# Optimization experiments

Hardware: AMD Instinct MI355X
Metric: run time of the kernel (lower is better)

Reference implementation:

```python
import jax, jax.numpy as jnp
import numpy as np

B, N, M = 64, 256, 16
ONF, OEF = 92, 41
NF, EF = 128, 64
FINAL = 128  # final_node_len; final_layer outputs FINAL//2


def _linear_params(key, fan_in, fan_out):
    # kaiming_uniform fan_in, relu: bound = sqrt(6/fan_in)
    bound = np.sqrt(6.0 / fan_in)
    W = jax.random.uniform(key, (fan_out, fan_in), jnp.float32, -bound, bound)
    b = jnp.zeros((fan_out,), jnp.float32)
    return W, b


def setup_inputs() -> dict:
    key = jax.random.key(0)
    ks = jax.random.split(key, 12)
    node_fea = jax.random.normal(ks[0], (B, N, ONF), jnp.float32)
    edge_fea = jax.random.normal(ks[1], (B, N, M, OEF), jnp.float32)
    edge_fea_idx = jax.random.randint(ks[2], (B, N, M), 0, N)
    dis = jax.random.uniform(ks[3], (N, N), jnp.float32)
    Wn, bn = _linear_params(ks[4], ONF, NF)
    We, be = _linear_params(ks[5], OEF, EF)
    W1, b1 = _linear_params(ks[6], 2 * NF + EF, 2 * NF)
    W2, b2 = _linear_params(ks[7], 2 * NF + EF, 2 * NF)
    W3, b3 = _linear_params(ks[8], 2 * NF + EF, 2 * NF)
    Wf, bf = _linear_params(ks[9], NF, FINAL // 2)
    return dict(node_fea=node_fea, edge_fea=edge_fea, edge_fea_idx=edge_fea_idx,
                dis=dis, Wn=Wn, bn=bn, We=We, be=be,
                W1=W1, b1=b1, a1=jnp.float32(0.7),
                W2=W2, b2=b2, a2=jnp.float32(0.7),
                W3=W3, b3=b3, a3=jnp.float32(0.7),
                Wf=Wf, bf=bf,
                DAw=jnp.float32(48.0 / 5.0), DAb=jnp.float32(-28.0 / 5.0))


def _conv(nf, ef, idx, W, b, alpha):
    # nf: [B,N,F]; ef: [B,N,M,E]; idx: [B,N,M]
    Bb, Nn, Mm = idx.shape
    F = nf.shape[-1]
    idx_c = jnp.maximum(idx, 0)
    gathered = jax.vmap(lambda x, i: x[i])(nf, idx_c)           # [B,N,M,F]
    self_exp = jnp.broadcast_to(nf[:, :, None, :], (Bb, Nn, Mm, F))
    total = jnp.concatenate([self_exp, gathered, ef], axis=-1)   # [B,N,M,2F+E]
    gated = jnp.einsum('bnmi,oi->bnmo', total, W) + b            # [B,N,M,2F]
    nbr_filter, nbr_core = jnp.split(gated, 2, axis=-1)
    mask = (idx >= 0).astype(nf.dtype)[..., None]
    nbr_filter = jax.nn.sigmoid(nbr_filter) * mask
    nbr_core = jax.nn.softplus(nbr_core)
    nbr_sumed = jnp.sum(nbr_filter * nbr_core, axis=2)           # [B,N,F]
    return jax.nn.softplus(alpha * nf + nbr_sumed)


def reference(node_fea, edge_fea, edge_fea_idx, dis,
              Wn, bn, We, be,
              W1, b1, a1, W2, b2, a2, W3, b3, a3,
              Wf, bf, DAw, DAb):
    nf = node_fea @ Wn.T + bn                                    # [B,N,NF]
    ef = edge_fea @ We.T + be                                    # [B,N,M,EF]
    nf = _conv(nf, ef, edge_fea_idx, W1, b1, a1)
    nf = _conv(nf, ef, edge_fea_idx, W2, b2, a2)
    nf = _conv(nf, ef, edge_fea_idx, W3, b3, a3)
    nf = nf @ Wf.T + bf                                          # [B,N,FINAL//2]
    DA = jax.nn.sigmoid(DAw * dis + DAb)                         # [N,N]
    node1 = jnp.einsum('ij,bjf->bif', DA, nf)
    return jnp.concatenate([nf, node1], axis=2)                  # [B,N,FINAL]
```

## Files before the change

### kernel.cpp

```cpp
#include <hip/hip_runtime.h>
#include <hip/hip_bf16.h>
#include <math.h>

#define Bb   64
#define Nn   256
#define Mm   16
#define ONF  92
#define OEF  41
#define NF   128
#define EF   64
#define KDIM 320
#define ODIM 256
#define FINAL 128
#define K0C  6

#define LOG2E_F 1.44269504088896f
#define LN2_F   0.6931471805599453f

typedef __attribute__((ext_vector_type(8))) short short8;
typedef __attribute__((ext_vector_type(4))) float f32x4;

__device__ __forceinline__ float sigmoidf_(float x) {
    float e = __expf(-x);
    return __builtin_amdgcn_rcpf(1.0f + e);
}
__device__ __forceinline__ float softplusf_(float x) {
    return fmaxf(x, 0.0f) + __logf(1.0f + __expf(-fabsf(x)));
}
__device__ __forceinline__ __hip_bfloat16 to_bf16(float x) { return __float2bfloat16(x); }

__device__ __forceinline__ void swz(const float* __restrict__ in, __hip_bfloat16* __restrict__ out,
                                    int t, int Itot, int koff, int Kuse, int K0, float scale)
{
    int j = t & 7;
    int u = t >> 3;
    int lane = u & 63;
    int ln16 = lane & 15, q = lane >> 4;
    int v = u >> 6;
    int k0 = v % K0, tile = v / K0;
    int n = tile * 16 + ln16, k = k0 * 32 + q * 8 + j;
    out[t] = (k < Kuse) ? to_bf16(scale * in[(size_t)n * Itot + koff + k]) : to_bf16(0.0f);
}

#define SZ_WET (OEF * EF)
#define SZ_WB  (16 * K0C * 512)
#define SZ_WS  (16 * 4 * 512)
#define SZ_WNB ((NF / 16) * 3 * 512)
#define SZ_WEB ((EF / 16) * 2 * 512)
#define SZ_WFB ((64 / 16) * 4 * 512)
#define SZ_DA  (Nn * Nn)
#define PREP_TOTAL (SZ_WET + 3 * SZ_WB + 3 * SZ_WS + SZ_WNB + SZ_WEB + SZ_WFB + SZ_DA)

__global__ __launch_bounds__(256) void k_prep(
    const float* __restrict__ We, const float* __restrict__ W1,
    const float* __restrict__ W2, const float* __restrict__ W3,
    const float* __restrict__ Wn, const float* __restrict__ Wf,
    const float* __restrict__ dis, const float* __restrict__ pw, const float* __restrict__ pb,
    float* __restrict__ WeT,
    __hip_bfloat16* __restrict__ W1b, __hip_bfloat16* __restrict__ W2b, __hip_bfloat16* __restrict__ W3b,
    __hip_bfloat16* __restrict__ W1s, __hip_bfloat16* __restrict__ W2s, __hip_bfloat16* __restrict__ W3s,
    __hip_bfloat16* __restrict__ Wnb, __hip_bfloat16* __restrict__ Web, __hip_bfloat16* __restrict__ Wfb,
    __hip_bfloat16* __restrict__ DAf)
{
    int t = blockIdx.x * 256 + threadIdx.x;
    if (t < SZ_WET) {
        int o = t / OEF, i = t - o * OEF;
        WeT[i * EF + o] = We[t];
        return;
    }
    t -= SZ_WET;
    if (t < SZ_WB) { swz(W1, W1b, t, KDIM, NF, 192, K0C, LOG2E_F); return; }
    t -= SZ_WB;
    if (t < SZ_WB) { swz(W2, W2b, t, KDIM, NF, 192, K0C, LOG2E_F); return; }
    t -= SZ_WB;
    if (t < SZ_WB) { swz(W3, W3b, t, KDIM, NF, 192, K0C, LOG2E_F); return; }
    t -= SZ_WB;
    if (t < SZ_WS) { swz(W1, W1s, t, KDIM, 0, NF, 4, LOG2E_F); return; }
    t -= SZ_WS;
    if (t < SZ_WS) { swz(W2, W2s, t, KDIM, 0, NF, 4, LOG2E_F); return; }
    t -= SZ_WS;
    if (t < SZ_WS) { swz(W3, W3s, t, KDIM, 0, NF, 4, LOG2E_F); return; }
    t -= SZ_WS;
    if (t < SZ_WNB) { swz(Wn, Wnb, t, ONF, 0, ONF, 3, 1.0f); return; }
    t -= SZ_WNB;
    if (t < SZ_WEB) { swz(We, Web, t, OEF, 0, OEF, 2, 1.0f); return; }
    t -= SZ_WEB;
    if (t < SZ_WFB) { swz(Wf, Wfb, t, NF, 0, NF, 4, 1.0f); return; }
    t -= SZ_WFB;
    if (t < SZ_DA) {
        int i = t >> 8, jx = t & 255;
        float v = sigmoidf_(fmaf(*pw, dis[t], *pb));
        int itile = i >> 4, ln16 = i & 15;
        int k0 = jx >> 5, q = (jx >> 3) & 3, jj = jx & 7;
        DAf[(size_t)((((itile * 8 + k0) << 6) + (q << 4) + ln16)) * 8 + jj] = to_bf16(v);
    }
}

template<int KIN, int K0, int NCOLS>
__device__ __forceinline__ void emb_body(
    int bid, const float* __restrict__ X, const __hip_bfloat16* __restrict__ Bswz,
    const float* __restrict__ bias, __hip_bfloat16* __restrict__ Y,
    __hip_bfloat16* A_s, __hip_bfloat16* O_s)
{
    constexpr int KP = K0 * 32;
    constexpr int TPW = NCOLS / 64;
    constexpr int OLD = NCOLS + 24;

    const int row0 = bid * 64;
    const int t = threadIdx.x;

    {
        const float4* Xb = (const float4*)(X + (size_t)row0 * KIN);
        constexpr int NV = (64 * KIN) / 4;
        for (int c = t; c < NV; c += 256) {
            float4 v = Xb[c];
            int flat = c * 4;
            #pragma unroll
            for (int e = 0; e < 4; e++) {
                int f = flat + e;
                int row = f / KIN, k = f - row * KIN;
                int mt = row >> 4, ln16 = row & 15;
                int k0 = k >> 5, q = (k >> 3) & 3, j = k & 7;
                float vv = (e == 0) ? v.x : (e == 1) ? v.y : (e == 2) ? v.z : v.w;
                A_s[(((mt * K0 + k0) << 6) + (q << 4) + ln16) * 8 + j] = to_bf16(vv);
            }
        }
        constexpr int PAD = KP - KIN;
        for (int c = t; c < 64 * PAD; c += 256) {
            int row = c / PAD, k = KIN + (c - row * PAD);
            int mt = row >> 4, ln16 = row & 15;
            int k0 = k >> 5, q = (k >> 3) & 3, j = k & 7;
            A_s[(((mt * K0 + k0) << 6) + (q << 4) + ln16) * 8 + j] = to_bf16(0.0f);
        }
    }
    __syncthreads();

    const int wv = t >> 6, lane = t & 63;
    const int q = lane >> 4, ln16 = lane & 15;

    f32x4 acc[4][TPW];
    #pragma unroll
    for (int p = 0; p < TPW; p++) {
        float bv = bias[(wv * TPW + p) * 16 + ln16];
        #pragma unroll
        for (int mt = 0; mt < 4; mt++) acc[mt][p] = (f32x4){bv, bv, bv, bv};
    }

    short8 bw[TPW][K0];
    #pragma unroll
    for (int p = 0; p < TPW; p++)
        #pragma unroll
        for (int k0 = 0; k0 < K0; k0++)
            bw[p][k0] = *(const short8*)(Bswz + ((size_t)((wv * TPW + p) * K0 + k0) << 9) + (lane << 3));

    #pragma unroll
    for (int k0 = 0; k0 < K0; k0++) {
        short8 af[4];
        #pragma unroll
        for (int mt = 0; mt < 4; mt++)
            af[mt] = *(const short8*)(A_s + (((mt * K0 + k0) << 6) + lane) * 8);
        #pragma unroll
        for (int mt = 0; mt < 4; mt++)
            #pragma unroll
            for (int p = 0; p < TPW; p++)
                acc[mt][p] = __builtin_amdgcn_mfma_f32_16x16x32_bf16(af[mt], bw[p][k0], acc[mt][p], 0, 0, 0);
    }

    #pragma unroll
    for (int mt = 0; mt < 4; mt++)
        #pragma unroll
        for (int p = 0; p < TPW; p++) {
            int col = (wv * TPW + p) * 16 + ln16;
            #pragma unroll
            for (int r = 0; r < 4; r++)
                O_s[(mt * 16 + q * 4 + r) * OLD + col] = to_bf16(acc[mt][p][r]);
        }
    __syncthreads();
    constexpr int CH = NCOLS / 8;
    for (int c = t; c < 64 * CH; c += 256) {
        int row = c / CH, ch = c - row * CH;
        *(uint4*)(Y + (size_t)(row0 + row) * NCOLS + ch * 8) =
            *(const uint4*)(O_s + row * OLD + ch * 8);
    }
}

__global__ __launch_bounds__(256) void k_embed_all(
    const float* __restrict__ node_fea, const __hip_bfloat16* __restrict__ Wnb,
    const float* __restrict__ bn, __hip_bfloat16* __restrict__ nf0,
    const float* __restrict__ edge_fea, const __hip_bfloat16* __restrict__ Web,
    const float* __restrict__ be, __hip_bfloat16* __restrict__ efb)
{
    __shared__ __align__(16) __hip_bfloat16 A_s[4 * 3 * 512];
    __shared__ __align__(16) __hip_bfloat16 O_s[64 * (NF + 24)];
    if (blockIdx.x < 256)
        emb_body<ONF, 3, NF>(blockIdx.x, node_fea, Wnb, bn, nf0, A_s, O_s);
    else
        emb_body<OEF, 2, EF>(blockIdx.x - 256, edge_fea, Web, be, efb, A_s, O_s);
}

template<bool PRECOMP>
__global__ __launch_bounds__(256, 3) void k_conv_mfma(
    const __hip_bfloat16* __restrict__ nf_in,
    const float* __restrict__ edge_fea,
    const __hip_bfloat16* __restrict__ ef_bf,
    const int*   __restrict__ eidx,
    const float* __restrict__ WeT,
    const float* __restrict__ be,
    const __hip_bfloat16* __restrict__ Wb,
    const __hip_bfloat16* __restrict__ Wsb,
    const float* __restrict__ bias,
    const float* __restrict__ palpha,
    __hip_bfloat16* __restrict__ nf_out)
{
    __shared__ __align__(16) __hip_bfloat16 A_s[4 * K0C * 512];
    __shared__ __align__(16) __hip_bfloat16 A_sf[4 * 512];

    const int node0 = blockIdx.x * 4;
    const int b = node0 >> 8;
    const int t = threadIdx.x;
    const int wv = t >> 6, lane = t & 63;
    const int q = lane >> 4, ln16 = lane & 15;
    const int row = (wv << 4) + ln16;

    const int myidx = eidx[node0 * Mm + row];
    const unsigned long long mball = __ballot(eidx[node0 * Mm + lane] >= 0);

    float selfv[8];
    #pragma unroll
    for (int mt = 0; mt < 4; mt++)
        #pragma unroll
        for (int p = 0; p < 2; p++)
            selfv[mt * 2 + p] =
                __bfloat162float(nf_in[(size_t)(node0 + mt) * NF + (2 * wv + p) * 16 + ln16]);

    {
        int j = myidx < 0 ? 0 : myidx;
        const __hip_bfloat16* gathp = nf_in + (size_t)((b << 8) + j) * NF;
        #pragma unroll
        for (int k0 = 0; k0 < 4; k0++)
            *(uint4*)(A_s + ((wv * K0C + k0) * 64 + lane) * 8) =
                *(const uint4*)(gathp + k0 * 32 + q * 8);
        *(uint4*)(A_sf + (wv * 64 + lane) * 8) =
            *(const uint4*)(nf_in + (size_t)(node0 + (ln16 & 3)) * NF + wv * 32 + q * 8);
        if (PRECOMP) {
            const __hip_bfloat16* efp = ef_bf + (size_t)((node0 << 4) + row) * EF;
            #pragma unroll
            for (int k0 = 0; k0 < 2; k0++)
                *(uint4*)(A_s + ((wv * K0C + 4 + k0) * 64 + lane) * 8) =
                    *(const uint4*)(efp + k0 * 32 + q * 8);
        } else {
            for (int c = t; c < 64 * EF; c += 256) {
                int rr = c >> 6, col = c & 63;
                float a = be[col];
                const float* er = edge_fea + (size_t)(node0 * Mm + rr) * OEF;
                #pragma unroll
                for (int i = 0; i < OEF; i++) a = fmaf(er[i], WeT[i * EF + col], a);
                int mt = rr >> 4, l16 = rr & 15;
                int k0 = 4 + (col >> 5), qq = (col >> 3) & 3, jj = col & 7;
                A_s[((mt * K0C + k0) * 64 + qq * 16 + l16) * 8 + jj] = to_bf16(a);
            }
        }
    }
    __syncthreads();

    f32x4 sv[4];
    #pragma unroll
    for (int c = 0; c < 4; c++) {
        int tile = 2 * wv + (c & 1) + ((c >> 1) << 3);
        float bv = bias[tile * 16 + ln16] * LOG2E_F;
        sv[c] = (f32x4){bv, bv, bv, bv};
    }
    #pragma unroll
    for (int k0 = 0; k0 < 4; k0++) {
        short8 afs = *(const short8*)(A_sf + (k0 * 64 + lane) * 8);
        #pragma unroll
        for (int c = 0; c < 4; c++) {
            int tile = 2 * wv + (c & 1) + ((c >> 1) << 3);
            short8 bws = *(const short8*)(Wsb + ((size_t)(tile * 4 + k0) << 9) + (lane << 3));
            sv[c] = __builtin_amdgcn_mfma_f32_16x16x32_bf16(afs, bws, sv[c], 0, 0, 0);
        }
    }

    f32x4 accF[4][2], accC[4][2];
    #pragma unroll
    for (int mt = 0; mt < 4; mt++) {
        #pragma unroll
        for (int p = 0; p < 2; p++) {
            float vF = __shfl(sv[p][mt], ln16);
            float vC = __shfl(sv[2 + p][mt], ln16);
            accF[mt][p] = (f32x4){vF, vF, vF, vF};
            accC[mt][p] = (f32x4){vC, vC, vC, vC};
        }
    }

    const __hip_bfloat16* WF0 = Wb + ((size_t)(2 * wv) * (K0C * 512)) + (lane << 3);
    const __hip_bfloat16* WF1 = WF0 + K0C * 512;
    const __hip_bfloat16* WC0 = WF0 + 8 * (K0C * 512);
    const __hip_bfloat16* WC1 = WC0 + K0C * 512;

    #pragma unroll
    for (int k0 = 0; k0 < K0C; k0++) {
        short8 cF0 = *(const short8*)(WF0 + k0 * 512);
        short8 cF1 = *(const short8*)(WF1 + k0 * 512);
        short8 cC0 = *(const short8*)(WC0 + k0 * 512);
        short8 cC1 = *(const short8*)(WC1 + k0 * 512);
        short8 af[4];
        #pragma unroll
        for (int mt = 0; mt < 4; mt++)
            af[mt] = *(const short8*)(A_s + ((mt * K0C + k0) * 64 + lane) * 8);
        #pragma unroll
        for (int mt = 0; mt < 4; mt++) {
            accF[mt][0] = __builtin_amdgcn_mfma_f32_16x16x32_bf16(af[mt], cF0, accF[mt][0], 0, 0, 0);
            accF[mt][1] = __builtin_amdgcn_mfma_f32_16x16x32_bf16(af[mt], cF1, accF[mt][1], 0, 0, 0);
            accC[mt][0] = __builtin_amdgcn_mfma_f32_16x16x32_bf16(af[mt], cC0, accC[mt][0], 0, 0, 0);
            accC[mt][1] = __builtin_amdgcn_mfma_f32_16x16x32_bf16(af[mt], cC1, accC[mt][1], 0, 0, 0);
        }
    }

    const float alpha = *palpha;
    #pragma unroll
    for (int mt = 0; mt < 4; mt++) {
        const int gnode = node0 + mt;
        unsigned mbits = (unsigned)(mball >> (mt * 16 + q * 4)) & 0xFu;
        #pragma unroll
        for (int p = 0; p < 2; p++) {
            float partial = 0.0f;
            #pragma unroll
            for (int r = 0; r < 4; r++) {
                bool msk = (mbits >> r) & 1u;
                float f2 = accF[mt][p][r];
                float c2 = accC[mt][p][r];
                float sig = __builtin_amdgcn_rcpf(1.0f + __builtin_amdgcn_exp2f(-f2));
                float sp2 = fmaxf(c2, 0.0f) +
                            __builtin_amdgcn_logf(1.0f + __builtin_amdgcn_exp2f(-fabsf(c2)));
                partial += msk ? sig * sp2 : 0.0f;
            }
            partial += __shfl_xor(partial, 16);
            partial += __shfl_xor(partial, 32);
            if (q == 0) {
                int col = (2 * wv + p) * 16 + ln16;
                nf_out[(size_t)gnode * NF + col] =
                    to_bf16(softplusf_(fmaf(alpha, selfv[mt * 2 + p], LN2_F * partial)));
            }
        }
    }
}

__global__ __launch_bounds__(256) void k_final_mfma(
    const __hip_bfloat16* __restrict__ nf, const __hip_bfloat16* __restrict__ Wfb,
    const float* __restrict__ bfv, float* __restrict__ out,
    __hip_bfloat16* __restrict__ XT)
{
    __shared__ __align__(16) __hip_bfloat16 A_s[16 * 512];
    const int node0 = blockIdx.x * 64;
    const int bloc = node0 >> 8;
    const int t = threadIdx.x;
    const int wv = t >> 6, lane = t & 63;
    const int q = lane >> 4, ln16 = lane & 15;

    const __hip_bfloat16* rowp = nf + (size_t)(node0 + (wv << 4) + ln16) * NF;
    #pragma unroll
    for (int k0 = 0; k0 < 4; k0++)
        *(uint4*)(A_s + ((wv * 4 + k0) * 64 + lane) * 8) =
            *(const uint4*)(rowp + k0 * 32 + q * 8);
    __syncthreads();

    short8 bw[4];
    #pragma unroll
    for (int k0 = 0; k0 < 4; k0++)
        bw[k0] = *(const short8*)(Wfb + ((size_t)(wv * 4 + k0) * 64 + lane) * 8);

    float bv = bfv[wv * 16 + ln16];
    f32x4 acc[4];
    #pragma unroll
    for (int mt = 0; mt < 4; mt++) acc[mt] = (f32x4){bv, bv, bv, bv};

    #pragma unroll
    for (int k0 = 0; k0 < 4; k0++) {
        short8 af[4];
        #pragma unroll
        for (int mt = 0; mt < 4; mt++)
            af[mt] = *(const short8*)(A_s + ((mt * 4 + k0) * 64 + lane) * 8);
        #pragma unroll
        for (int mt = 0; mt < 4; mt++)
            acc[mt] = __builtin_amdgcn_mfma_f32_16x16x32_bf16(af[mt], bw[k0], acc[mt], 0, 0, 0);
    }

    const int col = (wv << 4) + ln16;
    #pragma unroll
    for (int mt = 0; mt < 4; mt++)
        #pragma unroll
        for (int r = 0; r < 4; r++) {
            int row = mt * 16 + q * 4 + r;
            float v = acc[mt][r];
            out[(size_t)(node0 + row) * FINAL + col] = v;
            XT[(size_t)(bloc * 64 + col) * 256 + (node0 & 255) + row] = to_bf16(v);
        }
}

__global__ __launch_bounds__(256) void k_node1_mfma(
    const __hip_bfloat16* __restrict__ DAf,
    const __hip_bfloat16* __restrict__ XT,
    float* __restrict__ out)
{
    __shared__ __align__(16) __hip_bfloat16 B_s[32 * 512];
    const int blk = blockIdx.x;
    const int b = blk >> 2, i0 = (blk & 3) * 64;
    const int t = threadIdx.x;
    const int wv = t >> 6, lane = t & 63;
    const int q = lane >> 4, ln16 = lane & 15;

    const __hip_bfloat16* xrow = XT + (size_t)(b * 64 + (wv << 4) + ln16) * 256;
    #pragma unroll
    for (int k0 = 0; k0 < 8; k0++)
        *(uint4*)(B_s + ((wv * 8 + k0) * 64 + lane) * 8) =
            *(const uint4*)(xrow + k0 * 32 + q * 8);
    __syncthreads();

    f32x4 acc[4];
    #pragma unroll
    for (int mt = 0; mt < 4; mt++) acc[mt] = (f32x4){0.f, 0.f, 0.f, 0.f};

    #pragma unroll
    for (int k0 = 0; k0 < 8; k0++) {
        short8 bfr = *(const short8*)(B_s + ((wv * 8 + k0) * 64 + lane) * 8);
        short8 af[4];
        #pragma unroll
        for (int mt = 0; mt < 4; mt++)
            af[mt] = *(const short8*)(DAf + (size_t)(((i0 >> 4) + mt) * 8 + k0) * 512 + (lane << 3));
        #pragma unroll
        for (int mt = 0; mt < 4; mt++)
            acc[mt] = __builtin_amdgcn_mfma_f32_16x16x32_bf16(af[mt], bfr, acc[mt], 0, 0, 0);
    }

    #pragma unroll
    for (int mt = 0; mt < 4; mt++)
        #pragma unroll
        for (int r = 0; r < 4; r++) {
            int i = i0 + mt * 16 + q * 4 + r;
            out[(size_t)((b << 8) + i) * FINAL + 64 + (wv << 4) + ln16] = acc[mt][r];
        }
}

extern "C" void kernel_launch(void* const* d_in, const int* in_sizes, int n_in,
                              void* d_out, int out_size, void* d_ws, size_t ws_size,
                              hipStream_t stream)
{
    const float* node_fea = (const float*)d_in[0];
    const float* edge_fea = (const float*)d_in[1];
    const int*   eidx     = (const int*)  d_in[2];
    const float* dis      = (const float*)d_in[3];
    const float* Wn = (const float*)d_in[4];
    const float* bn = (const float*)d_in[5];
    const float* We = (const float*)d_in[6];
    const float* be = (const float*)d_in[7];
    const float* W1 = (const float*)d_in[8];
    const float* b1 = (const float*)d_in[9];
    const float* a1 = (const float*)d_in[10];
    const float* W2 = (const float*)d_in[11];
    const float* b2 = (const float*)d_in[12];
    const float* a2 = (const float*)d_in[13];
    const float* W3 = (const float*)d_in[14];
    const float* b3 = (const float*)d_in[15];
    const float* a3 = (const float*)d_in[16];
    const float* Wf = (const float*)d_in[17];
    const float* bf = (const float*)d_in[18];
    const float* DAw = (const float*)d_in[19];
    const float* DAb = (const float*)d_in[20];
    float* out = (float*)d_out;

    char* base = (char*)d_ws;
    size_t off = 0;
    auto alloc = [&](size_t bytes) { char* p = base + off; off = (off + bytes + 255) & ~(size_t)255; return p; };
    __hip_bfloat16* nfA = (__hip_bfloat16*)alloc((size_t)Bb * Nn * NF * 2);
    __hip_bfloat16* nfB = (__hip_bfloat16*)alloc((size_t)Bb * Nn * NF * 2);
    __hip_bfloat16* W1b = (__hip_bfloat16*)alloc((size_t)SZ_WB * 2);
    __hip_bfloat16* W2b = (__hip_bfloat16*)alloc((size_t)SZ_WB * 2);
    __hip_bfloat16* W3b = (__hip_bfloat16*)alloc((size_t)SZ_WB * 2);
    __hip_bfloat16* W1s = (__hip_bfloat16*)alloc((size_t)SZ_WS * 2);
    __hip_bfloat16* W2s = (__hip_bfloat16*)alloc((size_t)SZ_WS * 2);
    __hip_bfloat16* W3s = (__hip_bfloat16*)alloc((size_t)SZ_WS * 2);
    float* WeT = (float*)alloc((size_t)OEF * EF * 4);
    __hip_bfloat16* DAf = (__hip_bfloat16*)alloc((size_t)Nn * Nn * 2);
    __hip_bfloat16* Wnb = (__hip_bfloat16*)alloc((size_t)SZ_WNB * 2);
    __hip_bfloat16* Web = (__hip_bfloat16*)alloc((size_t)SZ_WEB * 2);
    __hip_bfloat16* Wfb = (__hip_bfloat16*)alloc((size_t)SZ_WFB * 2);
    __hip_bfloat16* XT  = (__hip_bfloat16*)alloc((size_t)Bb * 64 * Nn * 2);
    __hip_bfloat16* efb = (__hip_bfloat16*)alloc((size_t)Bb * Nn * Mm * EF * 2);
    const bool precomp = (ws_size >= off);

    hipLaunchKernelGGL(k_prep, dim3((PREP_TOTAL + 255) / 256), dim3(256), 0, stream,
                       We, W1, W2, W3, Wn, Wf, dis, DAw, DAb,
                       WeT, W1b, W2b, W3b, W1s, W2s, W3s, Wnb, Web, Wfb, DAf);

    hipLaunchKernelGGL(k_embed_all, dim3(precomp ? (256 + Bb * Nn * Mm / 64) : 256), dim3(256), 0, stream,
                       node_fea, Wnb, bn, nfA, edge_fea, Web, be, efb);

    if (precomp) {
        hipLaunchKernelGGL((k_conv_mfma<true>), dim3(Bb * Nn / 4), dim3(256), 0, stream,
                           nfA, edge_fea, efb, eidx, WeT, be, W1b, W1s, b1, a1, nfB);
        hipLaunchKernelGGL((k_conv_mfma<true>), dim3(Bb * Nn / 4), dim3(256), 0, stream,
                           nfB, edge_fea, efb, eidx, WeT, be, W2b, W2s, b2, a2, nfA);
        hipLaunchKernelGGL((k_conv_mfma<true>), dim3(Bb * Nn / 4), dim3(256), 0, stream,
                           nfA, edge_fea, efb, eidx, WeT, be, W3b, W3s, b3, a3, nfB);
    } else {
        hipLaunchKernelGGL((k_conv_mfma<false>), dim3(Bb * Nn / 4), dim3(256), 0, stream,
                           nfA, edge_fea, efb, eidx, WeT, be, W1b, W1s, b1, a1, nfB);
        hipLaunchKernelGGL((k_conv_mfma<false>), dim3(Bb * Nn / 4), dim3(256), 0, stream,
                           nfB, edge_fea, efb, eidx, WeT, be, W2b, W2s, b2, a2, nfA);
        hipLaunchKernelGGL((k_conv_mfma<false>), dim3(Bb * Nn / 4), dim3(256), 0, stream,
                           nfA, edge_fea, efb, eidx, WeT, be, W3b, W3s, b3, a3, nfB);
    }

    hipLaunchKernelGGL(k_final_mfma, dim3(Bb * Nn / 64), dim3(256), 0, stream, nfB, Wfb, bf, out, XT);
    hipLaunchKernelGGL(k_node1_mfma, dim3(Bb * 4), dim3(256), 0, stream, DAf, XT, out);
}
```

Baseline: 298.3 us.

## Add persistent multi-group conv kernel with register-resident weights and double-buffered LDS staging

```diff
diff --git a/kernel.cpp b/kernel.cpp
--- a/kernel.cpp
+++ b/kernel.cpp
@@ -13,12 +13,22 @@
 #define ODIM 256
 #define FINAL 128
 #define K0C  6
+#define GRP  8
+#define NODESB (4*GRP)
 
 #define LOG2E_F 1.44269504088896f
 #define LN2_F   0.6931471805599453f
 
 typedef __attribute__((ext_vector_type(8))) short short8;
 typedef __attribute__((ext_vector_type(4))) float f32x4;
+
+#define AS1 __attribute__((address_space(1)))
+#define AS3 __attribute__((address_space(3)))
+
+__device__ __forceinline__ void gl2lds16(const void* gp, void* lp) {
+    __builtin_amdgcn_global_load_lds((AS1 void*)(void*)gp, (AS3 void*)lp, 16, 0, 0);
+}
+#define KEEP8(x) asm volatile("" : "+v"(x))
 
 __device__ __forceinline__ float sigmoidf_(float x) {
     float e = __expf(-x);
@@ -198,6 +208,171 @@
         emb_body<OEF, 2, EF>(blockIdx.x - 256, edge_fea, Web, be, efb, A_s, O_s);
 }
 
+__global__ __launch_bounds__(256, 2) void k_conv_blk(
+    const __hip_bfloat16* __restrict__ nf_in,
+    const __hip_bfloat16* __restrict__ ef_bf,
+    const int*   __restrict__ eidx,
+    const __hip_bfloat16* __restrict__ Wb,
+    const __hip_bfloat16* __restrict__ Wsb,
+    const float* __restrict__ bias,
+    const float* __restrict__ palpha,
+    __hip_bfloat16* __restrict__ nf_out)
+{
+    __shared__ __align__(16) __hip_bfloat16 A_s[2][4 * K0C * 512];
+    __shared__ __align__(16) __hip_bfloat16 A_sf[8 * 512];
+
+    const int node0_blk = blockIdx.x * NODESB;
+    const int bbase = node0_blk & ~255;
+    const int t = threadIdx.x;
+    const int wv = t >> 6, lane = t & 63;
+    const int q = lane >> 4, ln16 = lane & 15;
+    const int row = (wv << 4) + ln16;
+    const float alpha = *palpha;
+
+    auto stage_group = [&](int node0g, __hip_bfloat16* buf) -> unsigned long long {
+        int mi = eidx[node0g * Mm + row];
+        unsigned long long mb = __ballot(eidx[node0g * Mm + lane] >= 0);
+        int j = mi < 0 ? 0 : mi;
+        const __hip_bfloat16* gathp = nf_in + (size_t)(bbase + j) * NF + q * 8;
+        #pragma unroll
+        for (int k0 = 0; k0 < 4; k0++)
+            gl2lds16(gathp + k0 * 32, buf + (wv * K0C + k0) * 512 + lane * 8);
+        const __hip_bfloat16* efp = ef_bf + (size_t)((node0g << 4) + row) * EF + q * 8;
+        #pragma unroll
+        for (int k0 = 0; k0 < 2; k0++)
+            gl2lds16(efp + k0 * 32, buf + (wv * K0C + 4 + k0) * 512 + lane * 8);
+        return mb;
+    };
+
+    {
+        const __hip_bfloat16* s0 = nf_in + (size_t)(node0_blk + ln16) * NF + wv * 32 + q * 8;
+        gl2lds16(s0, A_sf + wv * 512 + lane * 8);
+        gl2lds16(s0 + (size_t)16 * NF, A_sf + (4 + wv) * 512 + lane * 8);
+    }
+    unsigned long long mb_next = stage_group(node0_blk, A_s[0]);
+    __syncthreads();
+
+    const __hip_bfloat16* WF0 = Wb + ((size_t)(2 * wv) * (K0C * 512)) + (lane << 3);
+    const __hip_bfloat16* WF1 = WF0 + K0C * 512;
+    const __hip_bfloat16* WC0 = WF0 + 8 * (K0C * 512);
+    const __hip_bfloat16* WC1 = WC0 + K0C * 512;
+    short8 mF0[K0C], mF1[K0C], mC0[K0C], mC1[K0C];
+    #pragma unroll
+    for (int k0 = 0; k0 < K0C; k0++) {
+        mF0[k0] = *(const short8*)(WF0 + k0 * 512);
+        mF1[k0] = *(const short8*)(WF1 + k0 * 512);
+        mC0[k0] = *(const short8*)(WC0 + k0 * 512);
+        mC1[k0] = *(const short8*)(WC1 + k0 * 512);
+    }
+
+    f32x4 sv0[4], sv1[4];
+    #pragma unroll
+    for (int c = 0; c < 4; c++) {
+        int tile = 2 * wv + (c & 1) + ((c >> 1) << 3);
+        float bv = bias[tile * 16 + ln16] * LOG2E_F;
+        sv0[c] = (f32x4){bv, bv, bv, bv};
+        sv1[c] = (f32x4){bv, bv, bv, bv};
+    }
+    #pragma unroll
+    for (int k0 = 0; k0 < 4; k0++) {
+        short8 af0 = *(const short8*)(A_sf + (k0 * 64 + lane) * 8);
+        short8 af1 = *(const short8*)(A_sf + ((4 + k0) * 64 + lane) * 8);
+        #pragma unroll
+        for (int c = 0; c < 4; c++) {
+            int tile = 2 * wv + (c & 1) + ((c >> 1) << 3);
+            short8 bws = *(const short8*)(Wsb + ((size_t)(tile * 4 + k0) << 9) + (lane << 3));
+            sv0[c] = __builtin_amdgcn_mfma_f32_16x16x32_bf16(af0, bws, sv0[c], 0, 0, 0);
+            sv1[c] = __builtin_amdgcn_mfma_f32_16x16x32_bf16(af1, bws, sv1[c], 0, 0, 0);
+        }
+    }
+
+    #pragma unroll
+    for (int k0 = 0; k0 < K0C; k0++) {
+        KEEP8(mF0[k0]); KEEP8(mF1[k0]); KEEP8(mC0[k0]); KEEP8(mC1[k0]);
+    }
+
+    int cur = 0;
+    #pragma unroll 2
+    for (int g = 0; g < GRP; g++) {
+        const int node0g = node0_blk + g * 4;
+        const unsigned long long mb_cur = mb_next;
+        if (g + 1 < GRP) mb_next = stage_group(node0g + 4, A_s[cur ^ 1]);
+
+        float selfv[8];
+        #pragma unroll
+        for (int mt = 0; mt < 4; mt++)
+            #pragma unroll
+            for (int p = 0; p < 2; p++)
+                selfv[mt * 2 + p] =
+                    __bfloat162float(nf_in[(size_t)(node0g + mt) * NF + (2 * wv + p) * 16 + ln16]);
+
+        const bool gHi = (g >= 4);
+        const int srcl = ((g & 3) << 4) + ln16;
+        const __hip_bfloat16* Acur = A_s[cur];
+
+        #pragma unroll
+        for (int h = 0; h < 2; h++) {
+            f32x4 accF[2][2], accC[2][2];
+            #pragma unroll
+            for (int mtl = 0; mtl < 2; mtl++) {
+                const int mt = 2 * h + mtl;
+                #pragma unroll
+                for (int p = 0; p < 2; p++) {
+                    float sF = gHi ? sv1[p][mt]     : sv0[p][mt];
+                    float sC = gHi ? sv1[2 + p][mt] : sv0[2 + p][mt];
+                    float vF = __shfl(sF, srcl);
+                    float vC = __shfl(sC, srcl);
+                    accF[mtl][p] = (f32x4){vF, vF, vF, vF};
+                    accC[mtl][p] = (f32x4){vC, vC, vC, vC};
+                }
+            }
+            #pragma unroll
+            for (int k0 = 0; k0 < K0C; k0++) {
+                short8 af[2];
+                #pragma unroll
+                for (int mtl = 0; mtl < 2; mtl++)
+                    af[mtl] = *(const short8*)(Acur + (((2 * h + mtl) * K0C + k0) * 64 + lane) * 8);
+                #pragma unroll
+                for (int mtl = 0; mtl < 2; mtl++) {
+                    accF[mtl][0] = __builtin_amdgcn_mfma_f32_16x16x32_bf16(af[mtl], mF0[k0], accF[mtl][0], 0, 0, 0);
+                    accF[mtl][1] = __builtin_amdgcn_mfma_f32_16x16x32_bf16(af[mtl], mF1[k0], accF[mtl][1], 0, 0, 0);
+                    accC[mtl][0] = __builtin_amdgcn_mfma_f32_16x16x32_bf16(af[mtl], mC0[k0], accC[mtl][0], 0, 0, 0);
+                    accC[mtl][1] = __builtin_amdgcn_mfma_f32_16x16x32_bf16(af[mtl], mC1[k0], accC[mtl][1], 0, 0, 0);
+                }
+            }
+            #pragma unroll
+            for (int mtl = 0; mtl < 2; mtl++) {
+                const int mt = 2 * h + mtl;
+                const int gnode = node0g + mt;
+                unsigned mbits = (unsigned)(mb_cur >> (mt * 16 + q * 4)) & 0xFu;
+                #pragma unroll
+                for (int p = 0; p < 2; p++) {
+                    float partial = 0.0f;
+                    #pragma unroll
+                    for (int r = 0; r < 4; r++) {
+                        bool msk = (mbits >> r) & 1u;
+                        float f2 = accF[mtl][p][r];
+                        float c2 = accC[mtl][p][r];
+                        float sig = __builtin_amdgcn_rcpf(1.0f + __builtin_amdgcn_exp2f(-f2));
+                        float sp2 = fmaxf(c2, 0.0f) +
+                                    __builtin_amdgcn_logf(1.0f + __builtin_amdgcn_exp2f(-fabsf(c2)));
+                        partial += msk ? sig * sp2 : 0.0f;
+                    }
+                    partial += __shfl_xor(partial, 16);
+                    partial += __shfl_xor(partial, 32);
+                    if (q == 0) {
+                        int col = (2 * wv + p) * 16 + ln16;
+                        nf_out[(size_t)gnode * NF + col] =
+                            to_bf16(softplusf_(fmaf(alpha, selfv[mt * 2 + p], LN2_F * partial)));
+                    }
+                }
+            }
+        }
+        __syncthreads();
+        cur ^= 1;
+    }
+}
+
 template<bool PRECOMP>
 __global__ __launch_bounds__(256, 3) void k_conv_mfma(
     const __hip_bfloat16* __restrict__ nf_in,
@@ -497,12 +672,12 @@
                        node_fea, Wnb, bn, nfA, edge_fea, Web, be, efb);
 
     if (precomp) {
-        hipLaunchKernelGGL((k_conv_mfma<true>), dim3(Bb * Nn / 4), dim3(256), 0, stream,
-                           nfA, edge_fea, efb, eidx, WeT, be, W1b, W1s, b1, a1, nfB);
-        hipLaunchKernelGGL((k_conv_mfma<true>), dim3(Bb * Nn / 4), dim3(256), 0, stream,
-                           nfB, edge_fea, efb, eidx, WeT, be, W2b, W2s, b2, a2, nfA);
-        hipLaunchKernelGGL((k_conv_mfma<true>), dim3(Bb * Nn / 4), dim3(256), 0, stream,
-                           nfA, edge_fea, efb, eidx, WeT, be, W3b, W3s, b3, a3, nfB);
+        hipLaunchKernelGGL(k_conv_blk, dim3(Bb * Nn / NODESB), dim3(256), 0, stream,
+                           nfA, efb, eidx, W1b, W1s, b1, a1, nfB);
+        hipLaunchKernelGGL(k_conv_blk, dim3(Bb * Nn / NODESB), dim3(256), 0, stream,
+                           nfB, efb, eidx, W2b, W2s, b2, a2, nfA);
+        hipLaunchKernelGGL(k_conv_blk, dim3(Bb * Nn / NODESB), dim3(256), 0, stream,
+                           nfA, efb, eidx, W3b, W3s, b3, a3, nfB);
     } else {
         hipLaunchKernelGGL((k_conv_mfma<false>), dim3(Bb * Nn / 4), dim3(256), 0, stream,
                            nfA, edge_fea, efb, eidx, WeT, be, W1b, W1s, b1, a1, nfB);
```

Measured after the change: 291.5 us. 2.3% less time.

## Split conv linear into per-node projections plus per-edge edge GEMM

Applied to the files above, without the earlier changes.

```diff
diff --git a/kernel.cpp b/kernel.cpp
--- a/kernel.cpp
+++ b/kernel.cpp
@@ -19,6 +19,16 @@
 
 typedef __attribute__((ext_vector_type(8))) short short8;
 typedef __attribute__((ext_vector_type(4))) float f32x4;
+typedef unsigned int uint;
+typedef unsigned short ushort;
+
+#define AS1 __attribute__((address_space(1)))
+#define AS3 __attribute__((address_space(3)))
+
+__device__ __forceinline__ void gl2lds16(const void* gp, void* lp) {
+    __builtin_amdgcn_global_load_lds((AS1 void*)(void*)gp, (AS3 void*)lp, 16, 0, 0);
+}
+#define KEEP8(x) asm volatile("" : "+v"(x))
 
 __device__ __forceinline__ float sigmoidf_(float x) {
     float e = __expf(-x);
@@ -28,6 +38,12 @@
     return fmaxf(x, 0.0f) + __logf(1.0f + __expf(-fabsf(x)));
 }
 __device__ __forceinline__ __hip_bfloat16 to_bf16(float x) { return __float2bfloat16(x); }
+__device__ __forceinline__ float lo16(uint u) { return __uint_as_float(u << 16); }
+__device__ __forceinline__ float hi16(uint u) { return __uint_as_float(u & 0xffff0000u); }
+__device__ __forceinline__ ushort bfbits(float x) {
+    __hip_bfloat16 b = __float2bfloat16(x);
+    return *(ushort*)&b;
+}
 
 __device__ __forceinline__ void swz(const float* __restrict__ in, __hip_bfloat16* __restrict__ out,
                                     int t, int Itot, int koff, int Kuse, int K0, float scale)
@@ -45,11 +61,12 @@
 #define SZ_WET (OEF * EF)
 #define SZ_WB  (16 * K0C * 512)
 #define SZ_WS  (16 * 4 * 512)
+#define SZ_WE2 (16 * 2 * 512)
 #define SZ_WNB ((NF / 16) * 3 * 512)
 #define SZ_WEB ((EF / 16) * 2 * 512)
 #define SZ_WFB ((64 / 16) * 4 * 512)
 #define SZ_DA  (Nn * Nn)
-#define PREP_TOTAL (SZ_WET + 3 * SZ_WB + 3 * SZ_WS + SZ_WNB + SZ_WEB + SZ_WFB + SZ_DA)
+#define PREP_TOTAL (SZ_WET + 3 * SZ_WB + 3 * SZ_WS + SZ_WNB + SZ_WEB + SZ_WFB + 3 * SZ_WS + 3 * SZ_WE2 + SZ_DA)
 
 __global__ __launch_bounds__(256) void k_prep(
     const float* __restrict__ We, const float* __restrict__ W1,
@@ -60,6 +77,8 @@
     __hip_bfloat16* __restrict__ W1b, __hip_bfloat16* __restrict__ W2b, __hip_bfloat16* __restrict__ W3b,
     __hip_bfloat16* __restrict__ W1s, __hip_bfloat16* __restrict__ W2s, __hip_bfloat16* __restrict__ W3s,
     __hip_bfloat16* __restrict__ Wnb, __hip_bfloat16* __restrict__ Web, __hip_bfloat16* __restrict__ Wfb,
+    __hip_bfloat16* __restrict__ W1g, __hip_bfloat16* __restrict__ W2g, __hip_bfloat16* __restrict__ W3g,
+    __hip_bfloat16* __restrict__ W1e2, __hip_bfloat16* __restrict__ W2e2, __hip_bfloat16* __restrict__ W3e2,
     __hip_bfloat16* __restrict__ DAf)
 {
     int t = blockIdx.x * 256 + threadIdx.x;
@@ -87,6 +106,18 @@
     t -= SZ_WEB;
     if (t < SZ_WFB) { swz(Wf, Wfb, t, NF, 0, NF, 4, 1.0f); return; }
     t -= SZ_WFB;
+    if (t < SZ_WS) { swz(W1, W1g, t, KDIM, NF, NF, 4, LOG2E_F); return; }
+    t -= SZ_WS;
+    if (t < SZ_WS) { swz(W2, W2g, t, KDIM, NF, NF, 4, LOG2E_F); return; }
+    t -= SZ_WS;
+    if (t < SZ_WS) { swz(W3, W3g, t, KDIM, NF, NF, 4, LOG2E_F); return; }
+    t -= SZ_WS;
+    if (t < SZ_WE2) { swz(W1, W1e2, t, KDIM, 2 * NF, EF, 2, LOG2E_F); return; }
+    t -= SZ_WE2;
+    if (t < SZ_WE2) { swz(W2, W2e2, t, KDIM, 2 * NF, EF, 2, LOG2E_F); return; }
+    t -= SZ_WE2;
+    if (t < SZ_WE2) { swz(W3, W3e2, t, KDIM, 2 * NF, EF, 2, LOG2E_F); return; }
+    t -= SZ_WE2;
     if (t < SZ_DA) {
         int i = t >> 8, jx = t & 255;
         float v = sigmoidf_(fmaf(*pw, dis[t], *pb));
@@ -196,6 +227,177 @@
         emb_body<ONF, 3, NF>(blockIdx.x, node_fea, Wnb, bn, nf0, A_s, O_s);
     else
         emb_body<OEF, 2, EF>(blockIdx.x - 256, edge_fea, Web, be, efb, A_s, O_s);
+}
+
+__global__ __launch_bounds__(256) void k_gemm_p(
+    const __hip_bfloat16* __restrict__ nf,
+    const __hip_bfloat16* __restrict__ Ws,
+    const __hip_bfloat16* __restrict__ Wg,
+    const float* __restrict__ bias,
+    __hip_bfloat16* __restrict__ P)
+{
+    __shared__ __align__(16) __hip_bfloat16 A_s[8 * 512];
+    const int row0 = blockIdx.x * 32;
+    const int t = threadIdx.x;
+    const int wv = t >> 6, lane = t & 63;
+    const int q = lane >> 4, ln16 = lane & 15;
+
+    #pragma unroll
+    for (int cc = 0; cc < 2; cc++) {
+        int c = 2 * wv + cc;
+        int mt = c >> 2, k0 = c & 3;
+        gl2lds16(nf + (size_t)(row0 + mt * 16 + ln16) * NF + k0 * 32 + q * 8,
+                 (char*)A_s + (size_t)(c * 64 + lane) * 16);
+    }
+    __syncthreads();
+
+    const __hip_bfloat16* wbase = (wv < 2) ? Ws : Wg;
+    f32x4 acc[2][8];
+    #pragma unroll
+    for (int p = 0; p < 8; p++) {
+        float bv = (wv < 2) ? bias[(wv * 8 + p) * 16 + ln16] * LOG2E_F : 0.0f;
+        acc[0][p] = (f32x4){bv, bv, bv, bv};
+        acc[1][p] = (f32x4){bv, bv, bv, bv};
+    }
+
+    #pragma unroll
+    for (int k0 = 0; k0 < 4; k0++) {
+        short8 af0 = *(const short8*)(A_s + ((0 * 4 + k0) * 64 + lane) * 8);
+        short8 af1 = *(const short8*)(A_s + ((1 * 4 + k0) * 64 + lane) * 8);
+        #pragma unroll
+        for (int p = 0; p < 8; p++) {
+            int tt = (wv & 1) * 8 + p;
+            short8 bw = *(const short8*)(wbase + ((size_t)(tt * 4 + k0) << 9) + (lane << 3));
+            acc[0][p] = __builtin_amdgcn_mfma_f32_16x16x32_bf16(af0, bw, acc[0][p], 0, 0, 0);
+            acc[1][p] = __builtin_amdgcn_mfma_f32_16x16x32_bf16(af1, bw, acc[1][p], 0, 0, 0);
+        }
+    }
+
+    #pragma unroll
+    for (int mt = 0; mt < 2; mt++)
+        #pragma unroll
+        for (int p = 0; p < 8; p++) {
+            int col = (wv * 8 + p) * 16 + ln16;
+            #pragma unroll
+            for (int r = 0; r < 4; r++)
+                P[(size_t)(row0 + mt * 16 + q * 4 + r) * 512 + col] = to_bf16(acc[mt][p][r]);
+        }
+}
+
+__global__ __launch_bounds__(256, 3) void k_conv_p(
+    const __hip_bfloat16* __restrict__ nf_in,
+    const __hip_bfloat16* __restrict__ efb,
+    const int*   __restrict__ eidx,
+    const __hip_bfloat16* __restrict__ P,
+    const __hip_bfloat16* __restrict__ Wedge,
+    const float* __restrict__ palpha,
+    __hip_bfloat16* __restrict__ nf_out)
+{
+    __shared__ uint EG[64 * 129];
+    const int node0_blk = blockIdx.x * 16;
+    const int bbase = node0_blk & ~255;
+    const int t = threadIdx.x;
+    const int wv = t >> 6, lane = t & 63;
+    const int q = lane >> 4, ln16 = lane & 15;
+    const float alpha = *palpha;
+
+    short8 ws[4][2];
+    #pragma unroll
+    for (int c = 0; c < 4; c++) {
+        int ct = ((c >> 1) << 3) + 2 * wv + (c & 1);
+        #pragma unroll
+        for (int k0 = 0; k0 < 2; k0++)
+            ws[c][k0] = *(const short8*)(Wedge + ((size_t)(ct * 2 + k0) << 9) + (lane << 3));
+    }
+    #pragma unroll
+    for (int c = 0; c < 4; c++) { KEEP8(ws[c][0]); KEEP8(ws[c][1]); }
+
+    for (int g = 0; g < 4; g++) {
+        const int node0g = node0_blk + g * 4;
+
+        short8 bfr[4][2];
+        #pragma unroll
+        for (int et = 0; et < 4; et++)
+            #pragma unroll
+            for (int k0 = 0; k0 < 2; k0++)
+                bfr[et][k0] = *(const short8*)(
+                    efb + (size_t)((node0g + et) * 16 + ln16) * EF + k0 * 32 + q * 8);
+
+        f32x4 acc[4][4];
+        #pragma unroll
+        for (int et = 0; et < 4; et++)
+            #pragma unroll
+            for (int c = 0; c < 4; c++) acc[et][c] = (f32x4){0.f, 0.f, 0.f, 0.f};
+
+        #pragma unroll
+        for (int k0 = 0; k0 < 2; k0++)
+            #pragma unroll
+            for (int et = 0; et < 4; et++)
+                #pragma unroll
+                for (int c = 0; c < 4; c++)
+                    acc[et][c] = __builtin_amdgcn_mfma_f32_16x16x32_bf16(
+                        ws[c][k0], bfr[et][k0], acc[et][c], 0, 0, 0);
+
+        #pragma unroll
+        for (int et = 0; et < 4; et++) {
+            const int e = et * 16 + ln16;
+            #pragma unroll
+            for (int c = 0; c < 4; c++) {
+                int ct = ((c >> 1) << 3) + 2 * wv + (c & 1);
+                int wbase0 = e * 129 + ct * 8 + q * 2;
+                uint u0 = (uint)bfbits(acc[et][c][0]) | ((uint)bfbits(acc[et][c][1]) << 16);
+                uint u1 = (uint)bfbits(acc[et][c][2]) | ((uint)bfbits(acc[et][c][3]) << 16);
+                EG[wbase0] = u0;
+                EG[wbase0 + 1] = u1;
+            }
+        }
+        __syncthreads();
+
+        {
+            const int n = node0g + wv;
+            const uint* EGrow = EG + (wv * 16) * 129 + lane;
+            uint psF = *(const uint*)(P + (size_t)n * 512 + 2 * lane);
+            uint psC = *(const uint*)(P + (size_t)n * 512 + 128 + 2 * lane);
+            uint sfv = *(const uint*)(nf_in + (size_t)n * NF + 2 * lane);
+            float psFlo = lo16(psF), psFhi = hi16(psF);
+            float psClo = lo16(psC), psChi = hi16(psC);
+            float plo = 0.0f, phi = 0.0f;
+            const int4* ip = (const int4*)(eidx + n * Mm);
+            #pragma unroll
+            for (int mm = 0; mm < 4; mm++) {
+                int4 iv = ip[mm];
+                #pragma unroll
+                for (int k = 0; k < 4; k++) {
+                    int im = (k == 0) ? iv.x : (k == 1) ? iv.y : (k == 2) ? iv.z : iv.w;
+                    int m = mm * 4 + k;
+                    bool msk = im >= 0;
+                    int jm = msk ? im : 0;
+                    const __hip_bfloat16* pg = P + (size_t)(bbase + jm) * 512 + 256;
+                    uint pgF = *(const uint*)(pg + 2 * lane);
+                    uint pgC = *(const uint*)(pg + 128 + 2 * lane);
+                    uint egF = EGrow[m * 129];
+                    uint egC = EGrow[m * 129 + 64];
+                    float flo = lo16(egF) + lo16(pgF) + psFlo;
+                    float fhi = hi16(egF) + hi16(pgF) + psFhi;
+                    float clo = lo16(egC) + lo16(pgC) + psClo;
+                    float chi = hi16(egC) + hi16(pgC) + psChi;
+                    float slo = __builtin_amdgcn_rcpf(1.0f + __builtin_amdgcn_exp2f(-flo));
+                    float shi = __builtin_amdgcn_rcpf(1.0f + __builtin_amdgcn_exp2f(-fhi));
+                    float splo = fmaxf(clo, 0.0f) +
+                                 __builtin_amdgcn_logf(1.0f + __builtin_amdgcn_exp2f(-fabsf(clo)));
+                    float sphi = fmaxf(chi, 0.0f) +
+                                 __builtin_amdgcn_logf(1.0f + __builtin_amdgcn_exp2f(-fabsf(chi)));
+                    plo += msk ? slo * splo : 0.0f;
+                    phi += msk ? shi * sphi : 0.0f;
+                }
+            }
+            float outlo = softplusf_(fmaf(alpha, lo16(sfv), LN2_F * plo));
+            float outhi = softplusf_(fmaf(alpha, hi16(sfv), LN2_F * phi));
+            uint up = (uint)bfbits(outlo) | ((uint)bfbits(outhi) << 16);
+            *(uint*)(nf_out + (size_t)n * NF + 2 * lane) = up;
+        }
+        __syncthreads();
+    }
 }
 
 template<bool PRECOMP>
@@ -487,22 +689,36 @@
     __hip_bfloat16* Wfb = (__hip_bfloat16*)alloc((size_t)SZ_WFB * 2);
     __hip_bfloat16* XT  = (__hip_bfloat16*)alloc((size_t)Bb * 64 * Nn * 2);
     __hip_bfloat16* efb = (__hip_bfloat16*)alloc((size_t)Bb * Nn * Mm * EF * 2);
+    __hip_bfloat16* W1g = (__hip_bfloat16*)alloc((size_t)SZ_WS * 2);
+    __hip_bfloat16* W2g = (__hip_bfloat16*)alloc((size_t)SZ_WS * 2);
+    __hip_bfloat16* W3g = (__hip_bfloat16*)alloc((size_t)SZ_WS * 2);
+    __hip_bfloat16* W1e2 = (__hip_bfloat16*)alloc((size_t)SZ_WE2 * 2);
+    __hip_bfloat16* W2e2 = (__hip_bfloat16*)alloc((size_t)SZ_WE2 * 2);
+    __hip_bfloat16* W3e2 = (__hip_bfloat16*)alloc((size_t)SZ_WE2 * 2);
+    __hip_bfloat16* Pbuf = (__hip_bfloat16*)alloc((size_t)Bb * Nn * 512 * 2);
     const bool precomp = (ws_size >= off);
 
     hipLaunchKernelGGL(k_prep, dim3((PREP_TOTAL + 255) / 256), dim3(256), 0, stream,
                        We, W1, W2, W3, Wn, Wf, dis, DAw, DAb,
-                       WeT, W1b, W2b, W3b, W1s, W2s, W3s, Wnb, Web, Wfb, DAf);
+                       WeT, W1b, W2b, W3b, W1s, W2s, W3s, Wnb, Web, Wfb,
+                       W1g, W2g, W3g, W1e2, W2e2, W3e2, DAf);
 
     hipLaunchKernelGGL(k_embed_all, dim3(precomp ? (256 + Bb * Nn * Mm / 64) : 256), dim3(256), 0, stream,
                        node_fea, Wnb, bn, nfA, edge_fea, Web, be, efb);
 
     if (precomp) {
-        hipLaunchKernelGGL((k_conv_mfma<true>), dim3(Bb * Nn / 4), dim3(256), 0, stream,
-                           nfA, edge_fea, efb, eidx, WeT, be, W1b, W1s, b1, a1, nfB);
-        hipLaunchKernelGGL((k_conv_mfma<true>), dim3(Bb * Nn / 4), dim3(256), 0, stream,
-                           nfB, edge_fea, efb, eidx, WeT, be, W2b, W2s, b2, a2, nfA);
-        hipLaunchKernelGGL((k_conv_mfma<true>), dim3(Bb * Nn / 4), dim3(256), 0, stream,
-                           nfA, edge_fea, efb, eidx, WeT, be, W3b, W3s, b3, a3, nfB);
+        hipLaunchKernelGGL(k_gemm_p, dim3(Bb * Nn / 32), dim3(256), 0, stream,
+                           nfA, W1s, W1g, b1, Pbuf);
+        hipLaunchKernelGGL(k_conv_p, dim3(Bb * Nn / 16), dim3(256), 0, stream,
+                           nfA, efb, eidx, Pbuf, W1e2, a1, nfB);
+        hipLaunchKernelGGL(k_gemm_p, dim3(Bb * Nn / 32), dim3(256), 0, stream,
+                           nfB, W2s, W2g, b2, Pbuf);
+        hipLaunchKernelGGL(k_conv_p, dim3(Bb * Nn / 16), dim3(256), 0, stream,
+                           nfB, efb, eidx, Pbuf, W2e2, a2, nfA);
+        hipLaunchKernelGGL(k_gemm_p, dim3(Bb * Nn / 32), dim3(256), 0, stream,
+                           nfA, W3s, W3g, b3, Pbuf);
+        hipLaunchKernelGGL(k_conv_p, dim3(Bb * Nn / 16), dim3(256), 0, stream,
+                           nfA, efb, eidx, Pbuf, W3e2, a3, nfB);
     } else {
         hipLaunchKernelGGL((k_conv_mfma<false>), dim3(Bb * Nn / 4), dim3(256), 0, stream,
                            nfA, edge_fea, efb, eidx, WeT, be, W1b, W1s, b1, a1, nfB);
```

Result: slower. 387.9 us (+30.0%).
